# Kernel tuning notes

Hardware: AMD Instinct MI355X
Metric: run time of the kernel (lower is better)

## Reference

```python
import jax, jax.numpy as jnp
import numpy as np

N = 100000       # nodes
E = 3200000      # edges (avg degree 32)
F_IN = 256       # num_features
H = 128          # hidden_channels
C = 64           # num_classes
L = 16           # num_layers
ALPHA = 0.1
THETA = 0.5
# GCN2Conv: beta_l = log(theta / layer + 1), layer = 1..L
BETAS = [float(np.log(THETA / (l + 1) + 1.0)) for l in range(L)]


def setup_inputs() -> dict:
    key = jax.random.key(0)
    ks = jax.random.split(key, 8)
    x = jax.random.normal(ks[0], (N, F_IN), jnp.float32)
    edge_src = jax.random.randint(ks[1], (E,), 0, N)
    edge_dst = jax.random.randint(ks[2], (E,), 0, N)
    # pre-normalized adjacency weights (normalize=False in GCN2Conv), ~1/deg scale
    edge_weight = jax.random.uniform(ks[3], (E,), jnp.float32) / 32.0
    lin0_w = jax.random.normal(ks[4], (F_IN, H), jnp.float32) / np.sqrt(F_IN)
    lin0_b = jnp.zeros((H,), jnp.float32)
    lin1_w = jax.random.normal(ks[5], (H, C), jnp.float32) / np.sqrt(H)
    lin1_b = jnp.zeros((C,), jnp.float32)
    conv_w = jax.random.normal(ks[6], (L, H, H), jnp.float32) / np.sqrt(H)  # GCN2Conv weight1, no bias
    return dict(x=x, edge_src=edge_src, edge_dst=edge_dst, edge_weight=edge_weight,
                lin0_w=lin0_w, lin0_b=lin0_b, lin1_w=lin1_w, lin1_b=lin1_b, conv_w=conv_w)


def reference(x, edge_src, edge_dst, edge_weight, lin0_w, lin0_b, lin1_w, lin1_b, conv_w):
    # dropout p=0.0 -> identity
    x = jax.nn.relu(x @ lin0_w + lin0_b)  # [N, H]
    x0 = x
    for l in range(L):
        beta = BETAS[l]
        # SpMM: agg[i] = sum_{(j->i)} w * x[j]
        agg = jax.ops.segment_sum(edge_weight[:, None] * x[edge_src], edge_dst, num_segments=N)
        h = (1.0 - ALPHA) * agg + ALPHA * x0                      # initial residual mix
        h = (1.0 - beta) * h + beta * (h @ conv_w[l])             # identity mapping (shared_weights)
        x = jax.nn.relu(h + x)                                    # skip + relu
    return x @ lin1_w + lin1_b  # [N, C]
```

## Files before the change

### kernel.cpp

```cpp
#include <hip/hip_runtime.h>
#include <math.h>

#define NN 100000
#define NE 3200000
#define FIN 256
#define HH 128
#define CC 64
#define NL 16
#define NBLK 391

typedef unsigned short u16;
typedef unsigned int u32;
typedef short short8 __attribute__((ext_vector_type(8)));
typedef float f32x4 __attribute__((ext_vector_type(4)));
typedef float f32x2 __attribute__((ext_vector_type(2)));
typedef float float8 __attribute__((ext_vector_type(8)));

__device__ __forceinline__ float bf2f(u16 u) {
    u32 v = ((u32)u) << 16;
    return __builtin_bit_cast(float, v);
}
__device__ __forceinline__ u16 f2bf(float f) {
    u32 x = __builtin_bit_cast(u32, f);
    u32 lsb = (x >> 16) & 1;
    x += 0x7fffu + lsb;
    return (u16)(x >> 16);
}
__device__ __forceinline__ u32 pack2(float a, float b) {
    return (u32)f2bf(a) | ((u32)f2bf(b) << 16);
}


__global__ void hist_kernel(const int* __restrict__ edst, int* __restrict__ cp,
                            int* __restrict__ rank) {
    int e = blockIdx.x * 256 + threadIdx.x;
    if (e < NE) {
        int part = blockIdx.x & 7;
        int d = __builtin_nontemporal_load(&edst[e]);
        int r = atomicAdd(&cp[part * NN + d], 1);
        __builtin_nontemporal_store(r, &rank[e]);
    }
}

__global__ __launch_bounds__(256) void combine_kernel(int* __restrict__ cp,
                                                      int* __restrict__ counts) {
    int i = blockIdx.x * 256 + threadIdx.x;
    if (i < NN) {
        int s = 0;
#pragma unroll
        for (int p = 0; p < 8; ++p) {
            int v = cp[p * NN + i];
            cp[p * NN + i] = s;
            s += v;
        }
        counts[i] = s;
    }
}

__global__ __launch_bounds__(256) void scanA_kernel(const int* __restrict__ counts,
                                                    int* __restrict__ incl, int* __restrict__ bsum) {
    __shared__ int s[256];
    int t = threadIdx.x, i = blockIdx.x * 256 + t;
    s[t] = (i < NN) ? counts[i] : 0;
    __syncthreads();
    for (int off = 1; off < 256; off <<= 1) {
        int v = (t >= off) ? s[t - off] : 0;
        __syncthreads();
        s[t] += v;
        __syncthreads();
    }
    if (i < NN) incl[i] = s[t];
    if (t == 255) bsum[blockIdx.x] = s[255];
}

__global__ __launch_bounds__(512) void scanB_kernel(int* __restrict__ bsum) {
    __shared__ int s[512];
    int t = threadIdx.x;
    s[t] = (t < NBLK) ? bsum[t] : 0;
    __syncthreads();
    for (int off = 1; off < 512; off <<= 1) {
        int v = (t >= off) ? s[t - off] : 0;
        __syncthreads();
        s[t] += v;
        __syncthreads();
    }
    if (t < NBLK) bsum[t] = s[t];
}

__global__ __launch_bounds__(256) void scanC_kernel(const int* __restrict__ counts,
                                                    const int* __restrict__ incl,
                                                    const int* __restrict__ bsum,
                                                    int* __restrict__ row_start) {
    int t = threadIdx.x, b = blockIdx.x, i = b * 256 + t;
    if (i < NN) row_start[i] = (b ? bsum[b - 1] : 0) + incl[i] - counts[i];
    if (i == 0) row_start[NN] = NE;
}

__global__ void scatter_kernel(const int* __restrict__ esrc, const int* __restrict__ edst,
                               const float* __restrict__ ew, const int* __restrict__ row_start,
                               const int* __restrict__ rank, const int* __restrict__ cp,
                               u32* __restrict__ csr) {
    int e = blockIdx.x * 256 + threadIdx.x;
    if (e < NE) {
        int d = __builtin_nontemporal_load(&edst[e]);
        int sv = __builtin_nontemporal_load(&esrc[e]);
        float wv = __builtin_nontemporal_load(&ew[e]);
        int rk = __builtin_nontemporal_load(&rank[e]);
        int part = (e >> 8) & 7;
        int pos = row_start[d] + cp[part * NN + d] + rk;
        u32 wq = (u32)(wv * 1048544.0f + 0.5f);
        if (wq > 32767u) wq = 32767u;
        __builtin_nontemporal_store(((u32)sv << 15) | wq, &csr[pos]);
    }
}


__global__ void prep_kernel(const float* __restrict__ W0, const float* __restrict__ W1,
                            const float* __restrict__ CW, u16* __restrict__ Wfrag) {
    int f = blockIdx.x;
    int lane = threadIdx.x;
    const float* Wsrc;
    int KB, N, fl;
    float beta = -1.f;
    if (f < 64) { Wsrc = W0; KB = 8; N = 128; fl = f; }
    else if (f < 576) {
        int l = (f - 64) >> 5; fl = (f - 64) & 31;
        Wsrc = CW + (size_t)l * HH * HH; KB = 4; N = 128;
        beta = logf(0.5f / (float)(l + 1) + 1.0f);
    } else { Wsrc = W1; KB = 4; N = 64; fl = f - 576; }
    int j = fl / KB, k0 = fl % KB;
    int n = j * 16 + (lane & 15);
    u16* dst = Wfrag + (size_t)f * 512 + lane * 8;
#pragma unroll
    for (int i = 0; i < 8; ++i) {
        int k = k0 * 32 + ((lane >> 4) << 3) + i;
        float v = Wsrc[(size_t)k * N + n];
        if (beta >= 0.f) v = beta * v + ((k == n) ? (1.f - beta) : 0.f);
        dst[i] = f2bf(v);
    }
}


__global__ __launch_bounds__(256) void lin0_kernel(const float* __restrict__ X,
                                                   const u16* __restrict__ wf,
                                                   const float* __restrict__ B0,
                                                   u16* __restrict__ xcur,
                                                   u16* __restrict__ x0,
                                                   u32* __restrict__ xq) {
    __shared__ u16 cl[64 * 128];
    int t = threadIdx.x;
    int lane = t & 63, w = t >> 6;
    int nb = blockIdx.x * 64;
    int mb = nb + w * 16;
    int r = lane & 15, g = lane >> 4;
    int arow = mb + r; if (arow >= NN) arow = NN - 1;
    const float* aprow = X + (size_t)arow * FIN + g * 8;
    const short8* bp = (const short8*)wf + lane;
    f32x4 acc[8] = {};
#pragma unroll
    for (int k0 = 0; k0 < 8; ++k0) {
        float8 af = *(const float8*)(aprow + k0 * 32);
        short8 a;
#pragma unroll
        for (int i = 0; i < 8; ++i) a[i] = (short)f2bf(af[i]);
#pragma unroll
        for (int j = 0; j < 8; ++j)
            acc[j] = __builtin_amdgcn_mfma_f32_16x16x32_bf16(a, bp[(j * 8 + k0) * 64], acc[j], 0, 0, 0);
    }
#pragma unroll
    for (int j = 0; j < 8; ++j) {
        int col = j * 16 + r;
        float b = B0[col];
#pragma unroll
        for (int reg = 0; reg < 4; ++reg) {
            int lrow = w * 16 + g * 4 + reg;
            u32 idx = (u32)(lrow * 128 + col) ^ (u32)((lrow & 7) << 3);
            cl[idx] = f2bf(fmaxf(acc[j][reg] + b, 0.f));
        }
    }
    __syncthreads();
#pragma unroll
    for (int ppass = 0; ppass < 4; ++ppass) {
        int lrow = ppass * 16 + (t >> 4);
        int col0 = (t & 15) * 8;
        int grow = nb + lrow;
        if (grow < NN) {
            u32 idx = (u32)(lrow * 128 + col0) ^ (u32)((lrow & 7) << 3);
            short8 c = *(const short8*)&cl[idx];
            float o[8];
#pragma unroll
            for (int i = 0; i < 8; ++i) o[i] = fminf(bf2f((u16)c[i]), 448.f);
            *(short8*)(xcur + (size_t)grow * HH + col0) = c;
            *(short8*)(x0 + (size_t)grow * HH + col0) = c;
            u32 qa = 0, qb = 0;
            qa = __builtin_amdgcn_cvt_pk_fp8_f32(o[0], o[1], qa, false);
            qa = __builtin_amdgcn_cvt_pk_fp8_f32(o[2], o[3], qa, true);
            qb = __builtin_amdgcn_cvt_pk_fp8_f32(o[4], o[5], qb, false);
            qb = __builtin_amdgcn_cvt_pk_fp8_f32(o[6], o[7], qb, true);
            xq[(size_t)grow * 32 + (t & 15) * 2] = qa;
            xq[(size_t)grow * 32 + (t & 15) * 2 + 1] = qb;
        }
    }
}


__global__ __launch_bounds__(256) void spmm_kernel(const u16* __restrict__ xq16,
                                                   const u32* __restrict__ x0,
                                                   const u32* __restrict__ csr,
                                                   const int* __restrict__ row_start,
                                                   u32* __restrict__ h) {
    int node = blockIdx.x * 4 + (threadIdx.x >> 6);
    int d2 = threadIdx.x & 63;
    if (node >= NN) return;
    int p = row_start[node], pe = row_start[node + 1];
    float acc0 = 0.f, acc1 = 0.f;
    for (; p + 16 <= pe; p += 16) {
        u32 m[16];
#pragma unroll
        for (int q = 0; q < 16; ++q) m[q] = csr[p + q];
        u32 v[16];
#pragma unroll
        for (int q = 0; q < 16; ++q) v[q] = xq16[(size_t)(m[q] >> 15) * 64 + d2];
#pragma unroll
        for (int q = 0; q < 16; ++q) {
            f32x2 xv = __builtin_amdgcn_cvt_pk_f32_fp8(v[q], false);
            float wt = (float)(m[q] & 0x7fffu) * (1.0f / 1048544.0f);
            acc0 += wt * xv[0];
            acc1 += wt * xv[1];
        }
    }
    for (; p + 4 <= pe; p += 4) {
        u32 m[4];
#pragma unroll
        for (int q = 0; q < 4; ++q) m[q] = csr[p + q];
        u32 v[4];
#pragma unroll
        for (int q = 0; q < 4; ++q) v[q] = xq16[(size_t)(m[q] >> 15) * 64 + d2];
#pragma unroll
        for (int q = 0; q < 4; ++q) {
            f32x2 xv = __builtin_amdgcn_cvt_pk_f32_fp8(v[q], false);
            float wt = (float)(m[q] & 0x7fffu) * (1.0f / 1048544.0f);
            acc0 += wt * xv[0];
            acc1 += wt * xv[1];
        }
    }
    for (; p < pe; ++p) {
        u32 m = csr[p];
        f32x2 xv = __builtin_amdgcn_cvt_pk_f32_fp8((u32)xq16[(size_t)(m >> 15) * 64 + d2], false);
        float wt = (float)(m & 0x7fffu) * (1.0f / 1048544.0f);
        acc0 += wt * xv[0];
        acc1 += wt * xv[1];
    }
    int idx = node * 64 + d2;
    u32 xv = x0[idx];
    float r0 = 0.9f * acc0 + 0.1f * bf2f((u16)xv);
    float r1 = 0.9f * acc1 + 0.1f * bf2f((u16)(xv >> 16));
    h[idx] = pack2(r0, r1);
}


__global__ __launch_bounds__(256) void layer_kernel(const u16* __restrict__ h,
                                                    const u16* __restrict__ wf,
                                                    u16* __restrict__ x,
                                                    u32* __restrict__ xq) {
    __shared__ u16 cl[64 * 128];
    int t = threadIdx.x;
    int lane = t & 63, w = t >> 6;
    int nb = blockIdx.x * 64;
    int mb = nb + w * 16;
    int r = lane & 15, g = lane >> 4;
    int arow = mb + r; if (arow >= NN) arow = NN - 1;
    const short8* ap = (const short8*)(h + (size_t)arow * HH) + g;
    const short8* bp = (const short8*)wf + lane;
    f32x4 acc[8] = {};
#pragma unroll
    for (int k0 = 0; k0 < 4; ++k0) {
        short8 a = ap[k0 * 4];
#pragma unroll
        for (int j = 0; j < 8; ++j)
            acc[j] = __builtin_amdgcn_mfma_f32_16x16x32_bf16(a, bp[(j * 4 + k0) * 64], acc[j], 0, 0, 0);
    }
#pragma unroll
    for (int j = 0; j < 8; ++j) {
#pragma unroll
        for (int reg = 0; reg < 4; ++reg) {
            int lrow = w * 16 + g * 4 + reg;
            int col = j * 16 + r;
            u32 idx = (u32)(lrow * 128 + col) ^ (u32)((lrow & 7) << 3);
            cl[idx] = f2bf(acc[j][reg]);
        }
    }
    __syncthreads();
#pragma unroll
    for (int ppass = 0; ppass < 4; ++ppass) {
        int lrow = ppass * 16 + (t >> 4);
        int col0 = (t & 15) * 8;
        int grow = nb + lrow;
        if (grow < NN) {
            u32 idx = (u32)(lrow * 128 + col0) ^ (u32)((lrow & 7) << 3);
            short8 c = *(const short8*)&cl[idx];
            short8 sk = *(const short8*)(x + (size_t)grow * HH + col0);
            float o[8];
            short8 onew;
#pragma unroll
            for (int i = 0; i < 8; ++i) {
                float v = bf2f((u16)c[i]) + bf2f((u16)sk[i]);
                o[i] = fmaxf(v, 0.f);
                onew[i] = (short)f2bf(o[i]);
                o[i] = fminf(o[i], 448.f);
            }
            *(short8*)(x + (size_t)grow * HH + col0) = onew;
            u32 qa = 0, qb = 0;
            qa = __builtin_amdgcn_cvt_pk_fp8_f32(o[0], o[1], qa, false);
            qa = __builtin_amdgcn_cvt_pk_fp8_f32(o[2], o[3], qa, true);
            qb = __builtin_amdgcn_cvt_pk_fp8_f32(o[4], o[5], qb, false);
            qb = __builtin_amdgcn_cvt_pk_fp8_f32(o[6], o[7], qb, true);
            xq[(size_t)grow * 32 + (t & 15) * 2] = qa;
            xq[(size_t)grow * 32 + (t & 15) * 2 + 1] = qb;
        }
    }
}


__global__ __launch_bounds__(256) void lin1_kernel(const u16* __restrict__ x,
                                                   const u16* __restrict__ wf,
                                                   const float* __restrict__ B1,
                                                   float* __restrict__ out) {
    int lane = threadIdx.x & 63, w = threadIdx.x >> 6;
    int mb = (blockIdx.x * 4 + w) * 16;
    int r = lane & 15, g = lane >> 4;
    int arow = mb + r; if (arow >= NN) arow = NN - 1;
    const short8* ap = (const short8*)(x + (size_t)arow * HH) + g;
    const short8* bp = (const short8*)wf + lane;
    f32x4 acc[4] = {};
#pragma unroll
    for (int k0 = 0; k0 < 4; ++k0) {
        short8 a = ap[k0 * 4];
#pragma unroll
        for (int j = 0; j < 4; ++j)
            acc[j] = __builtin_amdgcn_mfma_f32_16x16x32_bf16(a, bp[(j * 4 + k0) * 64], acc[j], 0, 0, 0);
    }
#pragma unroll
    for (int j = 0; j < 4; ++j) {
        int col = j * 16 + r;
        float b = B1[col];
#pragma unroll
        for (int reg = 0; reg < 4; ++reg) {
            int row = mb + g * 4 + reg;
            if (row < NN) out[(size_t)row * CC + col] = acc[j][reg] + b;
        }
    }
}


extern "C" void kernel_launch(void* const* d_in, const int* in_sizes, int n_in,
                              void* d_out, int out_size, void* d_ws, size_t ws_size,
                              hipStream_t stream) {
    const float* X  = (const float*)d_in[0];
    const int* esrc = (const int*)d_in[1];
    const int* edst = (const int*)d_in[2];
    const float* ew = (const float*)d_in[3];
    const float* W0 = (const float*)d_in[4];
    const float* B0 = (const float*)d_in[5];
    const float* W1 = (const float*)d_in[6];
    const float* B1 = (const float*)d_in[7];
    const float* CW = (const float*)d_in[8];
    float* out = (float*)d_out;

    char* p = (char*)d_ws;
    auto alloc = [&](size_t bytes) {
        char* r = p;
        p += (bytes + 255) & ~(size_t)255;
        return r;
    };
    u16*   xcur      = (u16*)alloc((size_t)NN * HH * 2);
    u16*   x0        = (u16*)alloc((size_t)NN * HH * 2);
    u16*   hbuf      = (u16*)alloc((size_t)NN * HH * 2);
    u32*   xq        = (u32*)alloc((size_t)NN * 32 * 4);
    int*   row_start = (int*)alloc((size_t)(NN + 1) * 4);
    int*   counts    = (int*)alloc((size_t)NN * 4);
    int*   incl      = (int*)alloc((size_t)NN * 4);
    int*   bsum      = (int*)alloc((size_t)512 * 4);
    int*   cp        = (int*)alloc((size_t)8 * NN * 4);
    int*   rank      = (int*)alloc((size_t)NE * 4);
    u32*   csr       = (u32*)alloc((size_t)NE * 4);
    u16*   Wfrag     = (u16*)alloc((size_t)592 * 512 * 2);

    hipMemsetAsync(cp, 0, (size_t)8 * NN * 4, stream);
    hist_kernel<<<NE / 256, 256, 0, stream>>>(edst, cp, rank);
    combine_kernel<<<NBLK, 256, 0, stream>>>(cp, counts);
    scanA_kernel<<<NBLK, 256, 0, stream>>>(counts, incl, bsum);
    scanB_kernel<<<1, 512, 0, stream>>>(bsum);
    scanC_kernel<<<NBLK, 256, 0, stream>>>(counts, incl, bsum, row_start);
    scatter_kernel<<<NE / 256, 256, 0, stream>>>(esrc, edst, ew, row_start, rank, cp, csr);
    prep_kernel<<<592, 64, 0, stream>>>(W0, W1, CW, Wfrag);

    lin0_kernel<<<(NN + 63) / 64, 256, 0, stream>>>(X, Wfrag, B0, xcur, x0, xq);

    for (int l = 0; l < NL; ++l) {
        spmm_kernel<<<(NN + 3) / 4, 256, 0, stream>>>((const u16*)xq, (const u32*)x0,
                                                      csr, row_start, (u32*)hbuf);
        layer_kernel<<<(NN + 63) / 64, 256, 0, stream>>>(hbuf, Wfrag + (size_t)(64 + 32 * l) * 512,
                                                         xcur, xq);
    }

    lin1_kernel<<<(NN + 63) / 64, 256, 0, stream>>>(xcur, Wfrag + (size_t)576 * 512, B1, out);
}
```

Baseline: 1.800 ms.

## Pad CSR rows to multiples of 16 and drop SpMM tail loops

```diff
diff --git a/kernel.cpp b/kernel.cpp
--- a/kernel.cpp
+++ b/kernel.cpp
@@ -8,6 +8,7 @@
 #define CC 64
 #define NL 16
 #define NBLK 391
+#define NEPAD (NE + 16 * NN)
 
 typedef unsigned short u16;
 typedef unsigned int u32;
@@ -32,19 +33,23 @@
 
 
 __global__ void hist_kernel(const int* __restrict__ edst, int* __restrict__ cp,
-                            int* __restrict__ rank) {
+                            u16* __restrict__ rank) {
     int e = blockIdx.x * 256 + threadIdx.x;
     if (e < NE) {
         int part = blockIdx.x & 7;
         int d = __builtin_nontemporal_load(&edst[e]);
         int r = atomicAdd(&cp[part * NN + d], 1);
-        __builtin_nontemporal_store(r, &rank[e]);
-    }
-}
-
-__global__ __launch_bounds__(256) void combine_kernel(int* __restrict__ cp,
-                                                      int* __restrict__ counts) {
-    int i = blockIdx.x * 256 + threadIdx.x;
+        __builtin_nontemporal_store((u16)r, &rank[e]);
+    }
+}
+
+__global__ __launch_bounds__(256) void combine_scanA_kernel(int* __restrict__ cp,
+                                                            int* __restrict__ pcounts,
+                                                            int* __restrict__ incl,
+                                                            int* __restrict__ bsum) {
+    __shared__ int sh[256];
+    int t = threadIdx.x, b = blockIdx.x, i = b * 256 + t;
+    int padded = 0;
     if (i < NN) {
         int s = 0;
 #pragma unroll
@@ -53,24 +58,19 @@
             cp[p * NN + i] = s;
             s += v;
         }
-        counts[i] = s;
-    }
-}
-
-__global__ __launch_bounds__(256) void scanA_kernel(const int* __restrict__ counts,
-                                                    int* __restrict__ incl, int* __restrict__ bsum) {
-    __shared__ int s[256];
-    int t = threadIdx.x, i = blockIdx.x * 256 + t;
-    s[t] = (i < NN) ? counts[i] : 0;
+        padded = (s + 15) & ~15;
+        pcounts[i] = padded;
+    }
+    sh[t] = padded;
     __syncthreads();
     for (int off = 1; off < 256; off <<= 1) {
-        int v = (t >= off) ? s[t - off] : 0;
+        int v = (t >= off) ? sh[t - off] : 0;
         __syncthreads();
-        s[t] += v;
+        sh[t] += v;
         __syncthreads();
     }
-    if (i < NN) incl[i] = s[t];
-    if (t == 255) bsum[blockIdx.x] = s[255];
+    if (i < NN) incl[i] = sh[t];
+    if (t == 255) bsum[b] = sh[255];
 }
 
 __global__ __launch_bounds__(512) void scanB_kernel(int* __restrict__ bsum) {
@@ -87,25 +87,25 @@
     if (t < NBLK) bsum[t] = s[t];
 }
 
-__global__ __launch_bounds__(256) void scanC_kernel(const int* __restrict__ counts,
+__global__ __launch_bounds__(256) void scanC_kernel(const int* __restrict__ pcounts,
                                                     const int* __restrict__ incl,
                                                     const int* __restrict__ bsum,
                                                     int* __restrict__ row_start) {
     int t = threadIdx.x, b = blockIdx.x, i = b * 256 + t;
-    if (i < NN) row_start[i] = (b ? bsum[b - 1] : 0) + incl[i] - counts[i];
-    if (i == 0) row_start[NN] = NE;
+    if (i < NN) row_start[i] = (b ? bsum[b - 1] : 0) + incl[i] - pcounts[i];
+    if (i == 0) row_start[NN] = bsum[NBLK - 1];
 }
 
 __global__ void scatter_kernel(const int* __restrict__ esrc, const int* __restrict__ edst,
                                const float* __restrict__ ew, const int* __restrict__ row_start,
-                               const int* __restrict__ rank, const int* __restrict__ cp,
+                               const u16* __restrict__ rank, const int* __restrict__ cp,
                                u32* __restrict__ csr) {
     int e = blockIdx.x * 256 + threadIdx.x;
     if (e < NE) {
         int d = __builtin_nontemporal_load(&edst[e]);
         int sv = __builtin_nontemporal_load(&esrc[e]);
         float wv = __builtin_nontemporal_load(&ew[e]);
-        int rk = __builtin_nontemporal_load(&rank[e]);
+        int rk = rank[e];
         int part = (e >> 8) & 7;
         int pos = row_start[d] + cp[part * NN + d] + rk;
         u32 wq = (u32)(wv * 1048544.0f + 0.5f);
@@ -214,7 +214,7 @@
     if (node >= NN) return;
     int p = row_start[node], pe = row_start[node + 1];
     float acc0 = 0.f, acc1 = 0.f;
-    for (; p + 16 <= pe; p += 16) {
+    for (; p < pe; p += 16) {
         u32 m[16];
 #pragma unroll
         for (int q = 0; q < 16; ++q) m[q] = csr[p + q];
@@ -228,28 +228,6 @@
             acc0 += wt * xv[0];
             acc1 += wt * xv[1];
         }
-    }
-    for (; p + 4 <= pe; p += 4) {
-        u32 m[4];
-#pragma unroll
-        for (int q = 0; q < 4; ++q) m[q] = csr[p + q];
-        u32 v[4];
-#pragma unroll
-        for (int q = 0; q < 4; ++q) v[q] = xq16[(size_t)(m[q] >> 15) * 64 + d2];
-#pragma unroll
-        for (int q = 0; q < 4; ++q) {
-            f32x2 xv = __builtin_amdgcn_cvt_pk_f32_fp8(v[q], false);
-            float wt = (float)(m[q] & 0x7fffu) * (1.0f / 1048544.0f);
-            acc0 += wt * xv[0];
-            acc1 += wt * xv[1];
-        }
-    }
-    for (; p < pe; ++p) {
-        u32 m = csr[p];
-        f32x2 xv = __builtin_amdgcn_cvt_pk_f32_fp8((u32)xq16[(size_t)(m >> 15) * 64 + d2], false);
-        float wt = (float)(m & 0x7fffu) * (1.0f / 1048544.0f);
-        acc0 += wt * xv[0];
-        acc1 += wt * xv[1];
     }
     int idx = node * 64 + d2;
     u32 xv = x0[idx];
@@ -378,20 +356,20 @@
     u16*   hbuf      = (u16*)alloc((size_t)NN * HH * 2);
     u32*   xq        = (u32*)alloc((size_t)NN * 32 * 4);
     int*   row_start = (int*)alloc((size_t)(NN + 1) * 4);
-    int*   counts    = (int*)alloc((size_t)NN * 4);
+    int*   pcounts   = (int*)alloc((size_t)NN * 4);
     int*   incl      = (int*)alloc((size_t)NN * 4);
     int*   bsum      = (int*)alloc((size_t)512 * 4);
     int*   cp        = (int*)alloc((size_t)8 * NN * 4);
-    int*   rank      = (int*)alloc((size_t)NE * 4);
-    u32*   csr       = (u32*)alloc((size_t)NE * 4);
+    u16*   rank      = (u16*)alloc((size_t)NE * 2);
+    u32*   csr       = (u32*)alloc((size_t)NEPAD * 4);
     u16*   Wfrag     = (u16*)alloc((size_t)592 * 512 * 2);
 
     hipMemsetAsync(cp, 0, (size_t)8 * NN * 4, stream);
+    hipMemsetAsync(csr, 0, (size_t)NEPAD * 4, stream);
     hist_kernel<<<NE / 256, 256, 0, stream>>>(edst, cp, rank);
-    combine_kernel<<<NBLK, 256, 0, stream>>>(cp, counts);
-    scanA_kernel<<<NBLK, 256, 0, stream>>>(counts, incl, bsum);
+    combine_scanA_kernel<<<NBLK, 256, 0, stream>>>(cp, pcounts, incl, bsum);
     scanB_kernel<<<1, 512, 0, stream>>>(bsum);
-    scanC_kernel<<<NBLK, 256, 0, stream>>>(counts, incl, bsum, row_start);
+    scanC_kernel<<<NBLK, 256, 0, stream>>>(pcounts, incl, bsum, row_start);
     scatter_kernel<<<NE / 256, 256, 0, stream>>>(esrc, edst, ew, row_start, rank, cp, csr);
     prep_kernel<<<592, 64, 0, stream>>>(W0, W1, CW, Wfrag);
 
```

Measured after the change: 1.681 ms. 1.07x faster.
